# Performance work log

Hardware: AMD Instinct MI355X
Metric: run time of the kernel (lower is better)

## Reference

```python
import jax, jax.numpy as jnp
import numpy as np

N, D, H, E = 8192, 1024, 4096, 8


def setup_inputs() -> dict:
    key = jax.random.key(0)
    ks = jax.random.split(key, 5)
    s_in = 1.0 / np.sqrt(D)
    s_h = 1.0 / np.sqrt(H)
    return {
        "x": jax.random.normal(ks[0], (N, D), dtype=jnp.float32),
        "Wg": jax.random.normal(ks[1], (D, E), dtype=jnp.float32) * s_in,
        "bg": jnp.zeros((E,), dtype=jnp.float32),
        "W1": jax.random.normal(ks[2], (E, D, H), dtype=jnp.float32) * s_in,
        "b1": jnp.zeros((E, H), dtype=jnp.float32),
        "W2": jax.random.normal(ks[3], (E, H, D), dtype=jnp.float32) * s_h,
        "b2": jnp.zeros((E, D), dtype=jnp.float32),
    }


def reference(x, Wg, bg, W1, b1, W2, b2):
    # gate: softmax linear router -> weights [N, E]
    weights = jax.nn.softmax(x @ Wg + bg, axis=-1)
    # all experts, batched GEMMs: h [N, E, H]
    h = jax.nn.relu(jnp.einsum("nd,edh->neh", x, W1) + b1)  # Dropout is identity at inference
    outputs = jnp.einsum("neh,ehd->ned", h, W2) + b2         # [N, E, D]
    # weighted combine over experts
    return jnp.einsum("ne,ned->nd", weights, outputs)
```

## Files before the change

### kernel.cpp

```cpp
#include <hip/hip_runtime.h>
#include <hip/hip_bf16.h>

#define DDIM 1024
#define HDIM 4096
#define NEXP 8
#define NROW 8192

typedef __attribute__((ext_vector_type(8))) short s16x8;
typedef __attribute__((ext_vector_type(4))) float f32x4;

using bf16 = __hip_bfloat16;

__device__ __forceinline__ void gload16(const bf16* g, bf16* lds) {
    __builtin_amdgcn_global_load_lds(
        (const __attribute__((address_space(1))) unsigned int*)g,
        (__attribute__((address_space(3))) unsigned int*)lds,
        16, 0, 0);
}

template <int N>
__device__ __forceinline__ void wait_vmcnt() {
    if constexpr (N == 4)      asm volatile("s_waitcnt vmcnt(4)" ::: "memory");
    else if constexpr (N == 3) asm volatile("s_waitcnt vmcnt(3)" ::: "memory");
    else                       asm volatile("s_waitcnt vmcnt(0)" ::: "memory");
}

__global__ void cvt_x_kernel(const float* __restrict__ x, bf16* __restrict__ xb, int total4) {
    int i = blockIdx.x * 256 + threadIdx.x;
    if (i >= total4) return;
    float4 v = ((const float4*)x)[i];
    union { bf16 b[4]; uint2 u; } p;
    p.b[0] = __float2bfloat16(v.x);
    p.b[1] = __float2bfloat16(v.y);
    p.b[2] = __float2bfloat16(v.z);
    p.b[3] = __float2bfloat16(v.w);
    ((uint2*)xb)[i] = p.u;
}

__global__ void transpose_cvt_kernel(const float* __restrict__ in, bf16* __restrict__ out,
                                     int R, int C) {
    __shared__ float tile[32][33];
    const size_t esz = (size_t)R * C;
    const float* src = in + (size_t)blockIdx.z * esz;
    bf16* dst = out + (size_t)blockIdx.z * esz;
    int c0 = blockIdx.x * 32, r0 = blockIdx.y * 32;
    int tx = threadIdx.x & 31, ty = threadIdx.x >> 5;
#pragma unroll
    for (int i = 0; i < 32; i += 8)
        tile[ty + i][tx] = src[(size_t)(r0 + ty + i) * C + (c0 + tx)];
    __syncthreads();
#pragma unroll
    for (int i = 0; i < 32; i += 8)
        dst[(size_t)(c0 + ty + i) * R + (r0 + tx)] = __float2bfloat16(tile[tx][ty + i]);
}

__global__ void gate_kernel(const float* __restrict__ x, const float* __restrict__ Wg,
                            const float* __restrict__ bg, float* __restrict__ wts) {
    int wave = threadIdx.x >> 6, lane = threadIdx.x & 63;
    int n = blockIdx.x * 4 + wave;
    const float* xr = x + (size_t)n * DDIM;
    float acc[NEXP] = {0.f, 0.f, 0.f, 0.f, 0.f, 0.f, 0.f, 0.f};
    for (int d = lane; d < DDIM; d += 64) {
        float xv = xr[d];
        const float* wr = Wg + (size_t)d * NEXP;
#pragma unroll
        for (int e = 0; e < NEXP; ++e) acc[e] += xv * wr[e];
    }
#pragma unroll
    for (int off = 32; off > 0; off >>= 1) {
#pragma unroll
        for (int e = 0; e < NEXP; ++e) acc[e] += __shfl_xor(acc[e], off, 64);
    }
    if (lane == 0) {
        float mx = -1e30f;
#pragma unroll
        for (int e = 0; e < NEXP; ++e) { acc[e] += bg[e]; mx = fmaxf(mx, acc[e]); }
        float s = 0.f;
#pragma unroll
        for (int e = 0; e < NEXP; ++e) { acc[e] = __expf(acc[e] - mx); s += acc[e]; }
        float inv = 1.0f / s;
#pragma unroll
        for (int e = 0; e < NEXP; ++e) wts[(size_t)n * NEXP + e] = acc[e] * inv;
    }
}

__global__ void out_init_kernel(const float* __restrict__ wts, const float* __restrict__ b2,
                                float* __restrict__ out) {
    size_t idx = (size_t)blockIdx.x * 256 + threadIdx.x;
    int d = (int)(idx & (DDIM - 1));
    size_t n = idx >> 10;
    const float* w = wts + n * NEXP;
    float s = 0.f;
#pragma unroll
    for (int e = 0; e < NEXP; ++e) s += w[e] * b2[(size_t)e * DDIM + d];
    out[idx] = s;
}

template <int NR, int NPH, int MODE>
__global__ __launch_bounds__(512, 2) void gemm8(
    const bf16* __restrict__ A, const bf16* __restrict__ BT, void* __restrict__ Cout,
    const float* __restrict__ bias, const float* __restrict__ wts,
    int lda, int ldb, int ldc, int NT, int tilesM, int tilesN, int XGN, int expert) {
    constexpr int BN = NR * 32;
    constexpr int NRP = NR / NPH;
    constexpr int BIN = BN / 128;
    constexpr int LPT = 2 + BIN;
    constexpr int AELEMS = 256 * 32;
    constexpr int BELEMS = BN * 32;
    __shared__ __align__(16) bf16 lds[3][AELEMS + BELEMS];

    const int tid = threadIdx.x;
    const int wave = tid >> 6, lane = tid & 63;
    const int wm = wave >> 1, wn = wave & 1;
    const int r = lane & 15, kg = lane >> 4;

    const int xcd = blockIdx.x & 7, slot = blockIdx.x >> 3;
    const int XGM = 8 / XGN;
    const int rm = tilesM / XGM, rn = tilesN / XGN;
    const int g = slot >> 5, u = slot & 31;
    const int gpr = rn >> 3;
    const int gm = (g / gpr) * 4 + (u >> 3);
    const int gn = (g % gpr) * 8 + (u & 7);
    const int tm = (xcd / XGN) * rm + gm;
    const int tn = (xcd % XGN) * rn + gn;

    const bf16* gA = A + (size_t)tm * 256 * lda;
    const bf16* gB = BT + (size_t)tn * BN * ldb;

    f32x4 acc[4][NR];
#pragma unroll
    for (int m = 0; m < 4; ++m)
#pragma unroll
        for (int n = 0; n < NR; ++n) acc[m][n] = (f32x4){0.f, 0.f, 0.f, 0.f};

    auto stageA = [&](int t) {
        bf16* Ab = lds[t % 3];
#pragma unroll
        for (int j = 0; j < 2; ++j) {
            int c = j * 512 + tid;
            int R = c >> 2, kc = (c & 3) ^ ((R >> 1) & 3);
            gload16(gA + (size_t)R * lda + t * 32 + kc * 8, Ab + (j * 512 + wave * 64) * 8);
        }
    };
    auto stageB = [&](int t) {
        bf16* Bb = lds[t % 3] + AELEMS;
#pragma unroll
        for (int j = 0; j < BIN; ++j) {
            int c = j * 512 + tid;
            int R = c >> 2, kc = (c & 3) ^ ((R >> 1) & 3);
            gload16(gB + (size_t)R * ldb + t * 32 + kc * 8, Bb + (j * 512 + wave * 64) * 8);
        }
    };

    stageA(0); stageB(0);
    stageA(1); stageB(1);
    wait_vmcnt<LPT>();
    __builtin_amdgcn_s_barrier();

    for (int t = 0; t < NT; ++t) {
        const bf16* Ab = lds[t % 3];
        const bf16* Bb = Ab + AELEMS;
        s16x8 afr[4], bfr[NR];

#pragma unroll
        for (int m = 0; m < 4; ++m) {
            int R = wm * 64 + m * 16 + r;
            afr[m] = *(const s16x8*)(Ab + R * 32 + ((kg ^ ((R >> 1) & 3)) * 8));
        }
#pragma unroll
        for (int n = 0; n < NRP; ++n) {
            int R = wn * (NR * 16) + n * 16 + r;
            bfr[n] = *(const s16x8*)(Bb + R * 32 + ((kg ^ ((R >> 1) & 3)) * 8));
        }
        if (t + 2 < NT) stageA(t + 2);
        if (NPH == 1 && t + 2 < NT) stageB(t + 2);
        __builtin_amdgcn_s_barrier();
        asm volatile("s_waitcnt lgkmcnt(0)" ::: "memory");
        __builtin_amdgcn_sched_barrier(0);
        __builtin_amdgcn_s_setprio(1);
#pragma unroll
        for (int m = 0; m < 4; ++m)
#pragma unroll
            for (int n = 0; n < NRP; ++n)
                acc[m][n] = __builtin_amdgcn_mfma_f32_16x16x32_bf16(afr[m], bfr[n], acc[m][n], 0, 0, 0);
        __builtin_amdgcn_s_setprio(0);

        if (NPH == 2) {
            __builtin_amdgcn_s_barrier();
#pragma unroll
            for (int n = NRP; n < NR; ++n) {
                int R = wn * (NR * 16) + n * 16 + r;
                bfr[n] = *(const s16x8*)(Bb + R * 32 + ((kg ^ ((R >> 1) & 3)) * 8));
            }
            if (t + 2 < NT) stageB(t + 2);
            __builtin_amdgcn_s_barrier();
            asm volatile("s_waitcnt lgkmcnt(0)" ::: "memory");
            __builtin_amdgcn_sched_barrier(0);
            __builtin_amdgcn_s_setprio(1);
#pragma unroll
            for (int m = 0; m < 4; ++m)
#pragma unroll
                for (int n = NRP; n < NR; ++n)
                    acc[m][n] = __builtin_amdgcn_mfma_f32_16x16x32_bf16(afr[m], bfr[n], acc[m][n], 0, 0, 0);
            __builtin_amdgcn_s_setprio(0);
        }

        if (t + 1 < NT) {
            if (t + 2 < NT) wait_vmcnt<LPT>();
            else            wait_vmcnt<0>();
            __builtin_amdgcn_s_barrier();
        }
    }

    const size_t row0 = (size_t)tm * 256 + wm * 64;
    const int col0 = tn * BN + wn * (NR * 16);
    if (MODE == 1) {
        bf16* H = (bf16*)Cout;
#pragma unroll
        for (int n = 0; n < NR; ++n) {
            int cc = col0 + n * 16 + r;
            float bv = bias[cc];
#pragma unroll
            for (int m = 0; m < 4; ++m) {
#pragma unroll
                for (int j = 0; j < 4; ++j) {
                    size_t rr = row0 + m * 16 + kg * 4 + j;
                    float v = acc[m][n][j] + bv;
                    v = v > 0.f ? v : 0.f;
                    H[rr * (size_t)ldc + cc] = __float2bfloat16(v);
                }
            }
        }
    } else {
        float* O = (float*)Cout;
#pragma unroll
        for (int m = 0; m < 4; ++m) {
#pragma unroll
            for (int j = 0; j < 4; ++j) {
                size_t rr = row0 + m * 16 + kg * 4 + j;
                float wv = wts[rr * NEXP + expert];
#pragma unroll
                for (int n = 0; n < NR; ++n) {
                    int cc = col0 + n * 16 + r;
                    O[rr * (size_t)ldc + cc] += wv * acc[m][n][j];
                }
            }
        }
    }
}

extern "C" void kernel_launch(void* const* d_in, const int* in_sizes, int n_in,
                              void* d_out, int out_size, void* d_ws, size_t ws_size,
                              hipStream_t stream) {
    const float* x  = (const float*)d_in[0];
    const float* Wg = (const float*)d_in[1];
    const float* bg = (const float*)d_in[2];
    const float* W1 = (const float*)d_in[3];
    const float* b1 = (const float*)d_in[4];
    const float* W2 = (const float*)d_in[5];
    const float* b2 = (const float*)d_in[6];
    float* out = (float*)d_out;

    char* ws = (char*)d_ws;
    bf16* xb   = (bf16*)(ws);
    bf16* W1T  = (bf16*)(ws + (16ull << 20));
    bf16* W2T  = (bf16*)(ws + (80ull << 20));
    bf16* Hb   = (bf16*)(ws + (144ull << 20));
    float* wts = (float*)(ws + (208ull << 20));

    cvt_x_kernel<<<(NROW * DDIM / 4 + 255) / 256, 256, 0, stream>>>(x, xb, NROW * DDIM / 4);
    transpose_cvt_kernel<<<dim3(HDIM / 32, DDIM / 32, NEXP), 256, 0, stream>>>(W1, W1T, DDIM, HDIM);
    transpose_cvt_kernel<<<dim3(DDIM / 32, HDIM / 32, NEXP), 256, 0, stream>>>(W2, W2T, HDIM, DDIM);
    gate_kernel<<<NROW / 4, 256, 0, stream>>>(x, Wg, bg, wts);
    out_init_kernel<<<NROW * DDIM / 256, 256, 0, stream>>>(wts, b2, out);

    for (int e = 0; e < NEXP; ++e) {
        gemm8<8, 2, 1><<<512, 512, 0, stream>>>(
            xb, W1T + (size_t)e * HDIM * DDIM, Hb, b1 + (size_t)e * HDIM, nullptr,
            DDIM, DDIM, HDIM, DDIM / 32, 32, 16, 2, e);
        gemm8<4, 1, 2><<<256, 512, 0, stream>>>(
            Hb, W2T + (size_t)e * DDIM * HDIM, out, nullptr, wts,
            HDIM, HDIM, DDIM, HDIM / 32, 32, 8, 1, e);
    }
}
```

Measured before the change: 1.411 ms.

## Restructure expert GEMMs into 8-phase K=64 double-buffered pipeline with interleaved staging

Replaces the triple-buffered K=32 GEMM with a double-buffered K=64 design that splits each iteration into several LDS-read/MFMA phases, issuing global-to-LDS loads for later tiles between phases. The warp layout changes to 64x64-per-subtile with two M halves for the 256x256 tile, and occupancy drops to one block per CU (launch_bounds 512,1) to fit larger LDS and accumulators. The aim is to hide memory latency behind MFMA work with finer-grained interleaving, at the cost of occupancy and more barriers.

```diff
diff --git a/kernel.cpp b/kernel.cpp
--- a/kernel.cpp
+++ b/kernel.cpp
@@ -20,7 +20,7 @@
 
 template <int N>
 __device__ __forceinline__ void wait_vmcnt() {
-    if constexpr (N == 4)      asm volatile("s_waitcnt vmcnt(4)" ::: "memory");
+    if constexpr (N == 6)      asm volatile("s_waitcnt vmcnt(6)" ::: "memory");
     else if constexpr (N == 3) asm volatile("s_waitcnt vmcnt(3)" ::: "memory");
     else                       asm volatile("s_waitcnt vmcnt(0)" ::: "memory");
 }
@@ -96,22 +96,25 @@
     out[idx] = s;
 }
 
-template <int NR, int NPH, int MODE>
-__global__ __launch_bounds__(512, 2) void gemm8(
+template <int BN, int MODE>
+__global__ __launch_bounds__(512, 1) void gemm256(
     const bf16* __restrict__ A, const bf16* __restrict__ BT, void* __restrict__ Cout,
     const float* __restrict__ bias, const float* __restrict__ wts,
     int lda, int ldb, int ldc, int NT, int tilesM, int tilesN, int XGN, int expert) {
-    constexpr int BN = NR * 32;
-    constexpr int NRP = NR / NPH;
-    constexpr int BIN = BN / 128;
-    constexpr int LPT = 2 + BIN;
-    constexpr int AELEMS = 256 * 32;
-    constexpr int BELEMS = BN * 32;
-    __shared__ __align__(16) bf16 lds[3][AELEMS + BELEMS];
+    constexpr int WN = BN / 64, WM = 8 / WN;
+    constexpr int WROWS = 256 / WM;
+    constexpr int MH = WROWS / 64;
+    constexpr int HALFA = 256 * 32;
+    constexpr int HALFB = BN * 32;
+    constexpr int ATOT = 2 * HALFA;
+    constexpr int BUFE = ATOT + 2 * HALFB;
+    constexpr int BR = BN / 128;
+    constexpr int VMC = (BN == 256) ? 6 : 3;
+    __shared__ __align__(16) bf16 smem[2 * BUFE];
 
     const int tid = threadIdx.x;
     const int wave = tid >> 6, lane = tid & 63;
-    const int wm = wave >> 1, wn = wave & 1;
+    const int wm = wave / WN, wn = wave % WN;
     const int r = lane & 15, kg = lane >> 4;
 
     const int xcd = blockIdx.x & 7, slot = blockIdx.x >> 3;
@@ -127,105 +130,134 @@
     const bf16* gA = A + (size_t)tm * 256 * lda;
     const bf16* gB = BT + (size_t)tn * BN * ldb;
 
-    f32x4 acc[4][NR];
-#pragma unroll
-    for (int m = 0; m < 4; ++m)
-#pragma unroll
-        for (int n = 0; n < NR; ++n) acc[m][n] = (f32x4){0.f, 0.f, 0.f, 0.f};
-
-    auto stageA = [&](int t) {
-        bf16* Ab = lds[t % 3];
+    f32x4 acc[4 * MH][4];
+#pragma unroll
+    for (int m = 0; m < 4 * MH; ++m)
+#pragma unroll
+        for (int n = 0; n < 4; ++n) acc[m][n] = (f32x4){0.f, 0.f, 0.f, 0.f};
+
+    auto stageA = [&](int t, int ks) {
+        bf16* dst = smem + (t & 1) * BUFE + ks * HALFA;
 #pragma unroll
         for (int j = 0; j < 2; ++j) {
             int c = j * 512 + tid;
             int R = c >> 2, kc = (c & 3) ^ ((R >> 1) & 3);
-            gload16(gA + (size_t)R * lda + t * 32 + kc * 8, Ab + (j * 512 + wave * 64) * 8);
-        }
-    };
-    auto stageB = [&](int t) {
-        bf16* Bb = lds[t % 3] + AELEMS;
-#pragma unroll
-        for (int j = 0; j < BIN; ++j) {
+            gload16(gA + (size_t)R * lda + t * 64 + ks * 32 + kc * 8,
+                    dst + (j * 512 + wave * 64) * 8);
+        }
+    };
+    auto stageB = [&](int t, int ks) {
+        bf16* dst = smem + (t & 1) * BUFE + ATOT + ks * HALFB;
+#pragma unroll
+        for (int j = 0; j < BR; ++j) {
             int c = j * 512 + tid;
             int R = c >> 2, kc = (c & 3) ^ ((R >> 1) & 3);
-            gload16(gB + (size_t)R * ldb + t * 32 + kc * 8, Bb + (j * 512 + wave * 64) * 8);
-        }
-    };
-
-    stageA(0); stageB(0);
-    stageA(1); stageB(1);
-    wait_vmcnt<LPT>();
-    __builtin_amdgcn_s_barrier();
-
-    for (int t = 0; t < NT; ++t) {
-        const bf16* Ab = lds[t % 3];
-        const bf16* Bb = Ab + AELEMS;
-        s16x8 afr[4], bfr[NR];
-
+            gload16(gB + (size_t)R * ldb + t * 64 + ks * 32 + kc * 8,
+                    dst + (j * 512 + wave * 64) * 8);
+        }
+    };
+
+    s16x8 a0[4], bb[4];
+    auto ldA = [&](int buf, int ks, int mh) {
 #pragma unroll
         for (int m = 0; m < 4; ++m) {
-            int R = wm * 64 + m * 16 + r;
-            afr[m] = *(const s16x8*)(Ab + R * 32 + ((kg ^ ((R >> 1) & 3)) * 8));
-        }
-#pragma unroll
-        for (int n = 0; n < NRP; ++n) {
-            int R = wn * (NR * 16) + n * 16 + r;
-            bfr[n] = *(const s16x8*)(Bb + R * 32 + ((kg ^ ((R >> 1) & 3)) * 8));
-        }
-        if (t + 2 < NT) stageA(t + 2);
-        if (NPH == 1 && t + 2 < NT) stageB(t + 2);
+            int R = wm * WROWS + mh * 64 + m * 16 + r;
+            a0[m] = *(const s16x8*)&smem[buf * BUFE + ks * HALFA + R * 32 +
+                                         ((kg ^ ((R >> 1) & 3)) * 8)];
+        }
+    };
+    auto ldB = [&](int buf, int ks) {
+#pragma unroll
+        for (int n = 0; n < 4; ++n) {
+            int R = wn * 64 + n * 16 + r;
+            bb[n] = *(const s16x8*)&smem[buf * BUFE + ATOT + ks * HALFB + R * 32 +
+                                         ((kg ^ ((R >> 1) & 3)) * 8)];
+        }
+    };
+
+    auto preMFMA = [&]() {
         __builtin_amdgcn_s_barrier();
         asm volatile("s_waitcnt lgkmcnt(0)" ::: "memory");
         __builtin_amdgcn_sched_barrier(0);
         __builtin_amdgcn_s_setprio(1);
+    };
+    auto postMFMA = [&](bool vm) {
+        __builtin_amdgcn_s_setprio(0);
+        if (vm) wait_vmcnt<VMC>();
+        __builtin_amdgcn_s_barrier();
+    };
+    auto mfmaLo = [&]() {
 #pragma unroll
         for (int m = 0; m < 4; ++m)
 #pragma unroll
-            for (int n = 0; n < NRP; ++n)
-                acc[m][n] = __builtin_amdgcn_mfma_f32_16x16x32_bf16(afr[m], bfr[n], acc[m][n], 0, 0, 0);
-        __builtin_amdgcn_s_setprio(0);
-
-        if (NPH == 2) {
-            __builtin_amdgcn_s_barrier();
-#pragma unroll
-            for (int n = NRP; n < NR; ++n) {
-                int R = wn * (NR * 16) + n * 16 + r;
-                bfr[n] = *(const s16x8*)(Bb + R * 32 + ((kg ^ ((R >> 1) & 3)) * 8));
-            }
-            if (t + 2 < NT) stageB(t + 2);
-            __builtin_amdgcn_s_barrier();
-            asm volatile("s_waitcnt lgkmcnt(0)" ::: "memory");
-            __builtin_amdgcn_sched_barrier(0);
-            __builtin_amdgcn_s_setprio(1);
-#pragma unroll
-            for (int m = 0; m < 4; ++m)
-#pragma unroll
-                for (int n = NRP; n < NR; ++n)
-                    acc[m][n] = __builtin_amdgcn_mfma_f32_16x16x32_bf16(afr[m], bfr[n], acc[m][n], 0, 0, 0);
-            __builtin_amdgcn_s_setprio(0);
-        }
-
-        if (t + 1 < NT) {
-            if (t + 2 < NT) wait_vmcnt<LPT>();
-            else            wait_vmcnt<0>();
-            __builtin_amdgcn_s_barrier();
-        }
-    }
-
-    const size_t row0 = (size_t)tm * 256 + wm * 64;
-    const int col0 = tn * BN + wn * (NR * 16);
+            for (int n = 0; n < 4; ++n)
+                acc[m][n] = __builtin_amdgcn_mfma_f32_16x16x32_bf16(a0[m], bb[n], acc[m][n], 0, 0, 0);
+    };
+    auto mfmaHi = [&]() {
+#pragma unroll
+        for (int m = 0; m < 4; ++m)
+#pragma unroll
+            for (int n = 0; n < 4; ++n)
+                acc[4 + m][n] = __builtin_amdgcn_mfma_f32_16x16x32_bf16(a0[m], bb[n], acc[4 + m][n], 0, 0, 0);
+    };
+
+    if constexpr (MH == 2) {
+        stageB(0, 0); stageA(0, 0); stageB(0, 1); stageA(0, 1);
+        stageB(1, 0); stageA(1, 0); stageB(1, 1);
+    } else {
+        stageA(0, 0); stageB(0, 0); stageA(0, 1); stageB(0, 1);
+        stageA(1, 0); stageB(1, 0);
+    }
+    wait_vmcnt<VMC>();
+    __builtin_amdgcn_s_barrier();
+
+    const int NI = NT / 2;
+    for (int i = 0; i < NI; ++i) {
+        const int t0 = 2 * i, t1 = t0 + 1;
+        const bool g2 = (t0 + 2 < NT), g3 = (t1 + 2 < NT);
+        if constexpr (MH == 2) {
+            ldB(0, 0); ldA(0, 0, 0); stageA(t1, 1);
+            preMFMA(); mfmaLo(); postMFMA(false);
+            ldA(0, 0, 1); if (g2) stageB(t0 + 2, 0);
+            preMFMA(); mfmaHi(); postMFMA(false);
+            ldB(0, 1); ldA(0, 1, 0); if (g2) stageA(t0 + 2, 0);
+            preMFMA(); mfmaLo(); postMFMA(false);
+            ldA(0, 1, 1); if (g2) stageB(t0 + 2, 1);
+            preMFMA(); mfmaHi(); postMFMA(true);
+            ldB(1, 0); ldA(1, 0, 0); if (g2) stageA(t0 + 2, 1);
+            preMFMA(); mfmaLo(); postMFMA(false);
+            ldA(1, 0, 1); if (g3) stageB(t1 + 2, 0);
+            preMFMA(); mfmaHi(); postMFMA(false);
+            ldB(1, 1); ldA(1, 1, 0); if (g3) stageA(t1 + 2, 0);
+            preMFMA(); mfmaLo(); postMFMA(false);
+            ldA(1, 1, 1); if (g3) stageB(t1 + 2, 1);
+            preMFMA(); mfmaHi(); postMFMA(true);
+        } else {
+            ldB(0, 0); ldA(0, 0, 0); stageA(t1, 1); stageB(t1, 1);
+            preMFMA(); mfmaLo(); postMFMA(false);
+            ldB(0, 1); ldA(0, 1, 0); if (g2) { stageA(t0 + 2, 0); stageB(t0 + 2, 0); }
+            preMFMA(); mfmaLo(); postMFMA(true);
+            ldB(1, 0); ldA(1, 0, 0); if (g2) { stageA(t0 + 2, 1); stageB(t0 + 2, 1); }
+            preMFMA(); mfmaLo(); postMFMA(false);
+            ldB(1, 1); ldA(1, 1, 0); if (g3) { stageA(t1 + 2, 0); stageB(t1 + 2, 0); }
+            preMFMA(); mfmaLo(); postMFMA(true);
+        }
+    }
+
+    const size_t row0 = (size_t)tm * 256 + wm * WROWS;
+    const int col0 = tn * BN + wn * 64;
     if (MODE == 1) {
         bf16* H = (bf16*)Cout;
 #pragma unroll
-        for (int n = 0; n < NR; ++n) {
+        for (int n = 0; n < 4; ++n) {
             int cc = col0 + n * 16 + r;
             float bv = bias[cc];
 #pragma unroll
-            for (int m = 0; m < 4; ++m) {
+            for (int mf = 0; mf < 4 * MH; ++mf) {
 #pragma unroll
                 for (int j = 0; j < 4; ++j) {
-                    size_t rr = row0 + m * 16 + kg * 4 + j;
-                    float v = acc[m][n][j] + bv;
+                    size_t rr = row0 + (mf >> 2) * 64 + (mf & 3) * 16 + kg * 4 + j;
+                    float v = acc[mf][n][j] + bv;
                     v = v > 0.f ? v : 0.f;
                     H[rr * (size_t)ldc + cc] = __float2bfloat16(v);
                 }
@@ -234,15 +266,15 @@
     } else {
         float* O = (float*)Cout;
 #pragma unroll
-        for (int m = 0; m < 4; ++m) {
+        for (int mf = 0; mf < 4 * MH; ++mf) {
 #pragma unroll
             for (int j = 0; j < 4; ++j) {
-                size_t rr = row0 + m * 16 + kg * 4 + j;
+                size_t rr = row0 + (mf >> 2) * 64 + (mf & 3) * 16 + kg * 4 + j;
                 float wv = wts[rr * NEXP + expert];
 #pragma unroll
-                for (int n = 0; n < NR; ++n) {
+                for (int n = 0; n < 4; ++n) {
                     int cc = col0 + n * 16 + r;
-                    O[rr * (size_t)ldc + cc] += wv * acc[m][n][j];
+                    O[rr * (size_t)ldc + cc] += wv * acc[mf][n][j];
                 }
             }
         }
@@ -275,11 +307,11 @@
     out_init_kernel<<<NROW * DDIM / 256, 256, 0, stream>>>(wts, b2, out);
 
     for (int e = 0; e < NEXP; ++e) {
-        gemm8<8, 2, 1><<<512, 512, 0, stream>>>(
+        gemm256<256, 1><<<512, 512, 0, stream>>>(
             xb, W1T + (size_t)e * HDIM * DDIM, Hb, b1 + (size_t)e * HDIM, nullptr,
-            DDIM, DDIM, HDIM, DDIM / 32, 32, 16, 2, e);
-        gemm8<4, 1, 2><<<256, 512, 0, stream>>>(
+            DDIM, DDIM, HDIM, DDIM / 64, 32, 16, 2, e);
+        gemm256<128, 2><<<256, 512, 0, stream>>>(
             Hb, W2T + (size_t)e * DDIM * HDIM, out, nullptr, wts,
-            HDIM, HDIM, DDIM, HDIM / 32, 32, 8, 1, e);
-    }
-}
+            HDIM, HDIM, DDIM, HDIM / 64, 32, 8, 1, e);
+    }
+}
```

Result: slower. 1.501 ms (+6.4%).
